# Kernel tuning notes

Hardware: AMD Instinct MI355X
Metric: run time of the kernel (lower is better)

The kernel has to match this reference:

```python
import jax, jax.numpy as jnp
import numpy as np

B, S, H = 4, 2048, 1024
NH, HD = 16, 64
WIN = 64  # window_size = min(64, seq_len)
SCALE = float(np.sqrt(HD))


def setup_inputs() -> dict:
    key = jax.random.key(0)
    ks = jax.random.split(key, 10)
    w = lambda k, shp: (jax.random.normal(k, shp, jnp.float32) * 0.02)
    return {
        "x": jax.random.normal(ks[0], (B, S, H), jnp.float32),
        "attention_mask": jnp.ones((B, S), jnp.int32),
        "Wq": w(ks[1], (H, NH * HD)), "bq": jnp.zeros((NH * HD,), jnp.float32),
        "Wk": w(ks[2], (H, NH * HD)), "bk": jnp.zeros((NH * HD,), jnp.float32),
        "Wv": w(ks[3], (H, NH * HD)), "bv": jnp.zeros((NH * HD,), jnp.float32),
        "Wo": w(ks[4], (NH * HD, H)), "bo": jnp.zeros((H,), jnp.float32),
    }


def reference(x, attention_mask, Wq, bq, Wk, bk, Wv, bv, Wo, bo):
    # projections -> [B, NH, S, HD]
    def split_heads(t):
        return t.reshape(B, S, NH, HD).transpose(0, 2, 1, 3)
    q = split_heads(x @ Wq + bq)
    k = split_heads(x @ Wk + bk)
    v = split_heads(x @ Wv + bv)

    scores = jnp.einsum("bhqd,bhkd->bhqk", q, k) / SCALE  # [B,NH,S,S]

    # local banded mask: |i - j| <= window_size // 2
    idx = jnp.arange(S)
    local = jnp.abs(idx[None, :] - idx[:, None]) <= (WIN // 2)  # [S,S]
    scores = jnp.where(local[None, None, :, :], scores, -jnp.inf)

    # padding mask: [B,1,1,S]
    scores = jnp.where(attention_mask[:, None, None, :] == 0, -jnp.inf, scores)

    probs = jax.nn.softmax(scores, axis=-1)
    probs = jnp.nan_to_num(probs)  # rows that are fully masked -> 0

    out = jnp.einsum("bhqk,bhkd->bhqd", probs, v)
    out = out.transpose(0, 2, 1, 3).reshape(B, S, NH * HD)
    return out @ Wo + bo
```

## Files before the change

kernel.cpp:

```cpp
#include <hip/hip_runtime.h>
#include <stdint.h>

typedef unsigned short u16;
typedef __attribute__((ext_vector_type(8))) short short8;
typedef __attribute__((ext_vector_type(4))) float f32x4;

#define S_LEN 2048
#define HID   1024
#define QKV_LD 3072
#define M_ROWS 8192

__device__ __forceinline__ u16 f2bf(float f) {
  unsigned u = __float_as_uint(f);
  unsigned r = (u + 0x7fffu + ((u >> 16) & 1u)) >> 16;
  return (u16)r;
}

__device__ __forceinline__ void gload16(const u16* g, u16* l) {
  __builtin_amdgcn_global_load_lds(
      (const __attribute__((address_space(1))) unsigned int*)(g),
      (__attribute__((address_space(3))) unsigned int*)(l),
      16, 0, 0);
}

__device__ __forceinline__ void wgbar() {
  asm volatile("" ::: "memory");
  __builtin_amdgcn_s_barrier();
  asm volatile("" ::: "memory");
}

__global__ __launch_bounds__(256) void prep(
    const float* __restrict__ x, u16* __restrict__ xb,
    const float* __restrict__ bq, const float* __restrict__ bk,
    const float* __restrict__ bv, float* __restrict__ bqkv,
    const float* __restrict__ Wq, const float* __restrict__ Wk,
    const float* __restrict__ Wv, const float* __restrict__ Wo,
    u16* __restrict__ wqkvt, u16* __restrict__ wot) {
  __shared__ float tile[32][33];
  const int bid = blockIdx.x;
  if (bid < 4096) {
    int i = (bid * 256 + threadIdx.x) * 8;
    float4 a = *(const float4*)(x + i);
    float4 b = *(const float4*)(x + i + 4);
    u16 t[8];
    t[0] = f2bf(a.x); t[1] = f2bf(a.y); t[2] = f2bf(a.z); t[3] = f2bf(a.w);
    t[4] = f2bf(b.x); t[5] = f2bf(b.y); t[6] = f2bf(b.z); t[7] = f2bf(b.w);
    *(short8*)(xb + i) = *(short8*)t;
    return;
  }
  if (bid == 4096) {
    for (int i = threadIdx.x; i < 3072; i += 256)
      bqkv[i] = (i < 1024) ? bq[i] : (i < 2048) ? bk[i - 1024] : bv[i - 2048];
    return;
  }
  const int wid = bid - 4097;
  const int z = wid >> 10, rem = wid & 1023;
  const float* in = (z == 0) ? Wq : (z == 1) ? Wk : (z == 2) ? Wv : Wo;
  u16* out = (z < 3) ? (wqkvt + (size_t)z * 1024 * 1024) : wot;
  int tx = threadIdx.x & 31, ty = threadIdx.x >> 5;
  int n0 = (rem & 31) * 32, k0 = (rem >> 5) * 32;
#pragma unroll
  for (int i = 0; i < 32; i += 8)
    tile[ty + i][tx] = in[(size_t)(k0 + ty + i) * 1024 + n0 + tx];
  __syncthreads();
#pragma unroll
  for (int i = 0; i < 32; i += 8)
    out[(size_t)(n0 + ty + i) * 1024 + k0 + tx] = f2bf(tile[tx][ty + i]);
}

__global__ __launch_bounds__(512, 2) void gemm_k1(
    const u16* __restrict__ A, const u16* __restrict__ Bt,
    const float* __restrict__ bias, u16* __restrict__ C) {
  constexpr int K = 1024, NT = 16, N = 3072;
  constexpr int AU = 128 * 64;
  constexpr int SLAB = 320 * 64;
  __shared__ __align__(16) u16 smem[2 * SLAB];

  const int tid = threadIdx.x;
  const int wave = tid >> 6, lane = tid & 63;
  const int qlane = lane & 15, kgrp = lane >> 4;
  const int wm = wave >> 2, wn = wave & 3;
  int wg = blockIdx.x;
  wg = (wg & 7) * 128 + (wg >> 3);
  const int bm = wg >> 4, bn = wg & 15;

  const int srow = tid >> 3;
  const int sslot = (tid & 7) ^ (srow & 7);
  uint32_t gA[2], gB[3];
#pragma unroll
  for (int u = 0; u < 2; ++u)
    gA[u] = (uint32_t)((bm * 128 + u * 64 + srow) * K + sslot * 8);
#pragma unroll
  for (int u = 0; u < 3; ++u)
    gB[u] = (uint32_t)((bn * 192 + u * 64 + srow) * K + sslot * 8);

  auto stgA = [&](int t, int u) {
    gload16(A + (size_t)gA[u] + t * 64, &smem[(t & 1) * SLAB + u * 4096 + tid * 8]);
  };
  auto stgB = [&](int t, int u) {
    gload16(Bt + (size_t)gB[u] + t * 64, &smem[(t & 1) * SLAB + AU + u * 4096 + tid * 8]);
  };

  const int key7 = qlane & 7;
  int aaddr[4], baddr[3];
#pragma unroll
  for (int mf = 0; mf < 4; ++mf)
    aaddr[mf] = (wm * 64 + mf * 16 + qlane) * 64;
#pragma unroll
  for (int nf = 0; nf < 3; ++nf)
    baddr[nf] = AU + (wn * 48 + nf * 16 + qlane) * 64;

  f32x4 acc[4][3] = {};
  short8 af[4][2], bf[2][2];

  stgA(0, 0); stgA(0, 1);
  stgB(0, 0); stgB(0, 1); stgB(0, 2);
  stgA(1, 0); stgA(1, 1);
  asm volatile("s_waitcnt vmcnt(2)" ::: "memory");
  wgbar();

  for (int t = 0; t < NT; ++t) {
    const u16* bp = &smem[(t & 1) * SLAB];

#pragma unroll
    for (int mf = 0; mf < 4; ++mf)
#pragma unroll
      for (int kk = 0; kk < 2; ++kk)
        af[mf][kk] = *(const short8*)&bp[aaddr[mf] + (((kk * 4 + kgrp) ^ key7) * 8)];
#pragma unroll
    for (int nf = 0; nf < 2; ++nf)
#pragma unroll
      for (int kk = 0; kk < 2; ++kk)
        bf[nf][kk] = *(const short8*)&bp[baddr[nf] + (((kk * 4 + kgrp) ^ key7) * 8)];
    if (t + 1 < NT) { stgB(t + 1, 0); stgB(t + 1, 1); stgB(t + 1, 2); }
    wgbar();
    asm volatile("s_waitcnt lgkmcnt(0)" ::: "memory");
    __builtin_amdgcn_s_setprio(1);
#pragma unroll
    for (int mf = 0; mf < 4; ++mf)
#pragma unroll
      for (int nf = 0; nf < 2; ++nf)
#pragma unroll
        for (int kk = 0; kk < 2; ++kk)
          acc[mf][nf] = __builtin_amdgcn_mfma_f32_16x16x32_bf16(
              af[mf][kk], bf[nf][kk], acc[mf][nf], 0, 0, 0);
    __builtin_amdgcn_s_setprio(0);
    wgbar();

#pragma unroll
    for (int kk = 0; kk < 2; ++kk)
      bf[0][kk] = *(const short8*)&bp[baddr[2] + (((kk * 4 + kgrp) ^ key7) * 8)];
    if (t + 2 < NT) { stgA(t + 2, 0); stgA(t + 2, 1); }
    wgbar();
    asm volatile("s_waitcnt lgkmcnt(0)" ::: "memory");
    __builtin_amdgcn_s_setprio(1);
#pragma unroll
    for (int mf = 0; mf < 4; ++mf)
#pragma unroll
      for (int kk = 0; kk < 2; ++kk)
        acc[mf][2] = __builtin_amdgcn_mfma_f32_16x16x32_bf16(
            af[mf][kk], bf[0][kk], acc[mf][2], 0, 0, 0);
    __builtin_amdgcn_s_setprio(0);
    if (t + 2 < NT)      asm volatile("s_waitcnt vmcnt(2)" ::: "memory");
    else if (t + 1 < NT) asm volatile("s_waitcnt vmcnt(0)" ::: "memory");
    if (t + 1 < NT) wgbar();
  }

#pragma unroll
  for (int nf = 0; nf < 3; ++nf) {
    int col = bn * 192 + wn * 48 + nf * 16 + qlane;
    float bv = bias[col];
#pragma unroll
    for (int mf = 0; mf < 4; ++mf) {
      int row0 = bm * 128 + wm * 64 + mf * 16 + kgrp * 4;
#pragma unroll
      for (int r = 0; r < 4; ++r)
        C[(size_t)(row0 + r) * N + col] = f2bf(acc[mf][nf][r] + bv);
    }
  }
}

__global__ __launch_bounds__(256, 2) void gemm_k2(
    const u16* __restrict__ A, const u16* __restrict__ Bt,
    const float* __restrict__ bias, float* __restrict__ C) {
  constexpr int K = 1024, NT = 16, N = 1024;
  constexpr int AU = 128 * 64;
  constexpr int SLAB = 256 * 64;
  __shared__ __align__(16) u16 smem[2 * SLAB];

  const int tid = threadIdx.x;
  const int wave = tid >> 6, lane = tid & 63;
  const int qlane = lane & 15, kgrp = lane >> 4;
  const int wm = wave >> 1, wn = wave & 1;
  int wg = blockIdx.x;
  wg = (wg & 7) * 64 + (wg >> 3);
  const int bm = wg >> 3, bn = wg & 7;

  const int srow = tid >> 3;
  const int sslot = (tid & 7) ^ (srow & 7);
  uint32_t gA[4], gB[4];
#pragma unroll
  for (int u = 0; u < 4; ++u) {
    gA[u] = (uint32_t)((bm * 128 + u * 32 + srow) * K + sslot * 8);
    gB[u] = (uint32_t)((bn * 128 + u * 32 + srow) * K + sslot * 8);
  }
  auto stgA = [&](int t, int u) {
    gload16(A + (size_t)gA[u] + t * 64, &smem[(t & 1) * SLAB + u * 2048 + tid * 8]);
  };
  auto stgB = [&](int t, int u) {
    gload16(Bt + (size_t)gB[u] + t * 64, &smem[(t & 1) * SLAB + AU + u * 2048 + tid * 8]);
  };

  int aaddr[4], baddr[4];
#pragma unroll
  for (int f = 0; f < 4; ++f) {
    aaddr[f] = (wm * 64 + f * 16 + qlane) * 64;
    baddr[f] = AU + (wn * 64 + f * 16 + qlane) * 64;
  }
  const int arow7 = (wm * 64 + qlane) & 7;
  const int brow7 = (wn * 64 + qlane) & 7;

  f32x4 acc[4][4] = {};
  short8 af[4][2], bf[2][2];

#pragma unroll
  for (int u = 0; u < 4; ++u) stgA(0, u);
#pragma unroll
  for (int u = 0; u < 4; ++u) stgB(0, u);
#pragma unroll
  for (int u = 0; u < 4; ++u) stgA(1, u);
  stgB(1, 0); stgB(1, 2);
  asm volatile("s_waitcnt vmcnt(6)" ::: "memory");
  wgbar();

  for (int t = 0; t < NT; ++t) {
    const u16* bp = &smem[(t & 1) * SLAB];

#pragma unroll
    for (int mf = 0; mf < 4; ++mf)
#pragma unroll
      for (int kk = 0; kk < 2; ++kk)
        af[mf][kk] = *(const short8*)&bp[aaddr[mf] + (((kk * 4 + kgrp) ^ arow7) * 8)];
#pragma unroll
    for (int nf = 0; nf < 2; ++nf)
#pragma unroll
      for (int kk = 0; kk < 2; ++kk)
        bf[nf][kk] = *(const short8*)&bp[baddr[nf] + (((kk * 4 + kgrp) ^ brow7) * 8)];
    if (t + 1 < NT) { stgB(t + 1, 1); stgB(t + 1, 3); }
    wgbar();
    asm volatile("s_waitcnt lgkmcnt(0)" ::: "memory");
    __builtin_amdgcn_s_setprio(1);
#pragma unroll
    for (int mf = 0; mf < 4; ++mf)
#pragma unroll
      for (int nf = 0; nf < 2; ++nf)
#pragma unroll
        for (int kk = 0; kk < 2; ++kk)
          acc[mf][nf] = __builtin_amdgcn_mfma_f32_16x16x32_bf16(
              af[mf][kk], bf[nf][kk], acc[mf][nf], 0, 0, 0);
    __builtin_amdgcn_s_setprio(0);
    wgbar();

#pragma unroll
    for (int nf = 0; nf < 2; ++nf)
#pragma unroll
      for (int kk = 0; kk < 2; ++kk)
        bf[nf][kk] = *(const short8*)&bp[baddr[nf + 2] + (((kk * 4 + kgrp) ^ brow7) * 8)];
    if (t + 2 < NT) {
      stgA(t + 2, 0); stgA(t + 2, 1); stgA(t + 2, 2); stgA(t + 2, 3);
      stgB(t + 2, 0); stgB(t + 2, 2);
    }
    wgbar();
    asm volatile("s_waitcnt lgkmcnt(0)" ::: "memory");
    __builtin_amdgcn_s_setprio(1);
#pragma unroll
    for (int mf = 0; mf < 4; ++mf)
#pragma unroll
      for (int nf = 0; nf < 2; ++nf)
#pragma unroll
        for (int kk = 0; kk < 2; ++kk)
          acc[mf][nf + 2] = __builtin_amdgcn_mfma_f32_16x16x32_bf16(
              af[mf][kk], bf[nf][kk], acc[mf][nf + 2], 0, 0, 0);
    __builtin_amdgcn_s_setprio(0);
    if (t + 2 < NT)      asm volatile("s_waitcnt vmcnt(6)" ::: "memory");
    else if (t + 1 < NT) asm volatile("s_waitcnt vmcnt(0)" ::: "memory");
    if (t + 1 < NT) wgbar();
  }

#pragma unroll
  for (int nf = 0; nf < 4; ++nf) {
    int col = bn * 128 + wn * 64 + nf * 16 + qlane;
    float bv = bias[col];
#pragma unroll
    for (int mf = 0; mf < 4; ++mf) {
      int row0 = bm * 128 + wm * 64 + mf * 16 + kgrp * 4;
#pragma unroll
      for (int r = 0; r < 4; ++r)
        C[(size_t)(row0 + r) * N + col] = acc[mf][nf][r] + bv;
    }
  }
}

__global__ __launch_bounds__(256, 2) void attn_local(
    const u16* __restrict__ qkv, const int* __restrict__ amask,
    u16* __restrict__ aout) {
  __shared__ __align__(16) u16 Kl[192][72];
  __shared__ __align__(16) u16 Vt[64][200];
  __shared__ __align__(16) u16 Pl[4][32][104];

  const int tid = threadIdx.x, wave = tid >> 6, lane = tid & 63;
  const int qlane = lane & 15, kgrp = lane >> 4;
  const int rbz = blockIdx.x;
  const int bz = (rbz & 7) * 128 + (rbz >> 3);
  const int qt = bz & 15, h = (bz >> 4) & 15, b = bz >> 8;
  const int qs0 = qt * 128;
  const int jt = qs0 - 32;
  const size_t rbase = (size_t)b * S_LEN;

  {
    const int r0 = tid >> 3, c0 = (tid & 7) * 8;
#pragma unroll
    for (int p = 0; p < 6; ++p) {
      int row = p * 32 + r0;
      int j = jt + row;
      u16 kv[8], vv[8];
      if (j >= 0 && j < S_LEN) {
        const u16* kp = qkv + (rbase + j) * QKV_LD + HID + h * 64 + c0;
        *(short8*)kv = *(const short8*)kp;
        *(short8*)vv = *(const short8*)(kp + HID);
      } else {
#pragma unroll
        for (int q = 0; q < 8; ++q) { kv[q] = 0; vv[q] = 0; }
      }
      *(short8*)&Kl[row][c0] = *(short8*)kv;
#pragma unroll
      for (int q = 0; q < 8; ++q) Vt[c0 + q][row] = vv[q];
    }
  }

  short8 qf[2][2];
#pragma unroll
  for (int mf = 0; mf < 2; ++mf)
#pragma unroll
    for (int kk = 0; kk < 2; ++kk)
      qf[mf][kk] = *(const short8*)(qkv +
          (rbase + qs0 + wave * 32 + mf * 16 + qlane) * QKV_LD +
          h * 64 + kk * 32 + kgrp * 8);

  __syncthreads();

  f32x4 sc[2][6] = {};
#pragma unroll
  for (int kk = 0; kk < 2; ++kk) {
    short8 kf[6];
#pragma unroll
    for (int nf = 0; nf < 6; ++nf)
      kf[nf] = *(const short8*)&Kl[wave * 32 + nf * 16 + qlane][kk * 32 + kgrp * 8];
#pragma unroll
    for (int mf = 0; mf < 2; ++mf)
#pragma unroll
      for (int nf = 0; nf < 6; ++nf)
        sc[mf][nf] = __builtin_amdgcn_mfma_f32_16x16x32_bf16(
            qf[mf][kk], kf[nf], sc[mf][nf], 0, 0, 0);
  }

  int jcol[6], mv[6];
#pragma unroll
  for (int nf = 0; nf < 6; ++nf) {
    int j = jt + wave * 32 + nf * 16 + qlane;
    jcol[nf] = j;
    mv[nf] = (j >= 0 && j < S_LEN) ? amask[rbase + j] : 0;
  }

  float inv[2][4];
#pragma unroll
  for (int mf = 0; mf < 2; ++mf) {
    const int irow0 = qs0 + wave * 32 + mf * 16 + kgrp * 4;
    float mx[4] = {-1e30f, -1e30f, -1e30f, -1e30f};
#pragma unroll
    for (int r = 0; r < 4; ++r) {
      int i = irow0 + r;
#pragma unroll
      for (int nf = 0; nf < 6; ++nf) {
        int d = i - jcol[nf];
        if (mv[nf] && d >= -32 && d <= 32) mx[r] = fmaxf(mx[r], sc[mf][nf][r]);
      }
    }
#pragma unroll
    for (int m = 1; m < 16; m <<= 1)
#pragma unroll
      for (int r = 0; r < 4; ++r)
        mx[r] = fmaxf(mx[r], __shfl_xor(mx[r], m));
    float sm[4] = {0.f, 0.f, 0.f, 0.f};
#pragma unroll
    for (int r = 0; r < 4; ++r) {
      int i = irow0 + r;
#pragma unroll
      for (int nf = 0; nf < 6; ++nf) {
        int d = i - jcol[nf];
        bool val = mv[nf] && d >= -32 && d <= 32;
        float p = val ? __expf((sc[mf][nf][r] - mx[r]) * 0.125f) : 0.f;
        sc[mf][nf][r] = p;
        sm[r] += p;
      }
    }
#pragma unroll
    for (int m = 1; m < 16; m <<= 1)
#pragma unroll
      for (int r = 0; r < 4; ++r)
        sm[r] += __shfl_xor(sm[r], m);
#pragma unroll
    for (int r = 0; r < 4; ++r)
      inv[mf][r] = sm[r] > 0.f ? 1.f / sm[r] : 0.f;
#pragma unroll
    for (int nf = 0; nf < 6; ++nf)
#pragma unroll
      for (int r = 0; r < 4; ++r)
        Pl[wave][mf * 16 + kgrp * 4 + r][nf * 16 + qlane] = f2bf(sc[mf][nf][r]);
  }
  __syncthreads();

  f32x4 oc[2][4] = {};
#pragma unroll
  for (int ks = 0; ks < 3; ++ks) {
    short8 pa[2], vb[4];
#pragma unroll
    for (int mf = 0; mf < 2; ++mf)
      pa[mf] = *(const short8*)&Pl[wave][mf * 16 + qlane][ks * 32 + kgrp * 8];
#pragma unroll
    for (int nf = 0; nf < 4; ++nf)
      vb[nf] = *(const short8*)&Vt[nf * 16 + qlane][wave * 32 + ks * 32 + kgrp * 8];
#pragma unroll
    for (int mf = 0; mf < 2; ++mf)
#pragma unroll
      for (int nf = 0; nf < 4; ++nf)
        oc[mf][nf] = __builtin_amdgcn_mfma_f32_16x16x32_bf16(
            pa[mf], vb[nf], oc[mf][nf], 0, 0, 0);
  }

#pragma unroll
  for (int mf = 0; mf < 2; ++mf)
#pragma unroll
    for (int nf = 0; nf < 4; ++nf)
#pragma unroll
      for (int r = 0; r < 4; ++r) {
        size_t row = rbase + qs0 + wave * 32 + mf * 16 + kgrp * 4 + r;
        aout[row * HID + h * 64 + nf * 16 + qlane] =
            f2bf(oc[mf][nf][r] * inv[mf][r]);
      }
}

extern "C" void kernel_launch(void* const* d_in, const int* in_sizes, int n_in,
                              void* d_out, int out_size, void* d_ws, size_t ws_size,
                              hipStream_t stream) {
  const float* x  = (const float*)d_in[0];
  const int* amask = (const int*)d_in[1];
  const float* Wq = (const float*)d_in[2];
  const float* bq = (const float*)d_in[3];
  const float* Wk = (const float*)d_in[4];
  const float* bk = (const float*)d_in[5];
  const float* Wv = (const float*)d_in[6];
  const float* bv = (const float*)d_in[7];
  const float* Wo = (const float*)d_in[8];
  const float* bo = (const float*)d_in[9];
  float* out = (float*)d_out;

  char* w = (char*)d_ws;
  u16* xb    = (u16*)w;   w += (size_t)M_ROWS * HID * 2;
  u16* wqkvt = (u16*)w;   w += (size_t)3072 * 1024 * 2;
  u16* wot   = (u16*)w;   w += (size_t)1024 * 1024 * 2;
  float* bqkv = (float*)w; w += 3072 * 4 + 256;
  u16* qkv   = (u16*)w;   w += (size_t)M_ROWS * 3072 * 2;
  u16* aout  = (u16*)w;   w += (size_t)M_ROWS * HID * 2;

  prep<<<8193, 256, 0, stream>>>(x, xb, bq, bk, bv, bqkv,
                                 Wq, Wk, Wv, Wo, wqkvt, wot);
  gemm_k1<<<1024, 512, 0, stream>>>(xb, wqkvt, bqkv, qkv);
  attn_local<<<1024, 256, 0, stream>>>(qkv, amask, aout);
  gemm_k2<<<512, 256, 0, stream>>>(aout, wot, bo, out);
}
```

Measured before the change: 112.5 us.

## Enlarge QKV GEMM block tile to 256x192 with 4x2 wave layout

The QKV projection GEMM now computes a 256x192 output tile per workgroup instead of 128x192. Its 8 waves are arranged 4x2, and each wave owns a 64x96 sub-tile. The K-step is split into four MFMA phases using half-width fragments, and A staging grows to four loads per tile. This raises data reuse per LDS load and halves the grid to 512 blocks. In exchange it uses more LDS, with 448-row slabs double-buffered (about 114KB), which may limit occupancy to one block per CU. It also adds barriers and raises accumulator register pressure.

```diff
diff --git a/kernel.cpp b/kernel.cpp
--- a/kernel.cpp
+++ b/kernel.cpp
@@ -72,24 +72,24 @@
     const u16* __restrict__ A, const u16* __restrict__ Bt,
     const float* __restrict__ bias, u16* __restrict__ C) {
   constexpr int K = 1024, NT = 16, N = 3072;
-  constexpr int AU = 128 * 64;
-  constexpr int SLAB = 320 * 64;
+  constexpr int AU = 256 * 64;
+  constexpr int SLAB = 448 * 64;
   __shared__ __align__(16) u16 smem[2 * SLAB];
 
   const int tid = threadIdx.x;
   const int wave = tid >> 6, lane = tid & 63;
   const int qlane = lane & 15, kgrp = lane >> 4;
-  const int wm = wave >> 2, wn = wave & 3;
+  const int wm = wave >> 1, wn = wave & 1;
   int wg = blockIdx.x;
-  wg = (wg & 7) * 128 + (wg >> 3);
+  wg = (wg & 7) * 64 + (wg >> 3);
   const int bm = wg >> 4, bn = wg & 15;
 
   const int srow = tid >> 3;
   const int sslot = (tid & 7) ^ (srow & 7);
-  uint32_t gA[2], gB[3];
-#pragma unroll
-  for (int u = 0; u < 2; ++u)
-    gA[u] = (uint32_t)((bm * 128 + u * 64 + srow) * K + sslot * 8);
+  uint32_t gA[4], gB[3];
+#pragma unroll
+  for (int u = 0; u < 4; ++u)
+    gA[u] = (uint32_t)((bm * 256 + u * 64 + srow) * K + sslot * 8);
 #pragma unroll
   for (int u = 0; u < 3; ++u)
     gB[u] = (uint32_t)((bn * 192 + u * 64 + srow) * K + sslot * 8);
@@ -102,21 +102,26 @@
   };
 
   const int key7 = qlane & 7;
-  int aaddr[4], baddr[3];
+  const int s0 = (kgrp ^ key7) * 8;
+  const int s1 = ((4 + kgrp) ^ key7) * 8;
+  int aaddr[4], baddr[6];
 #pragma unroll
   for (int mf = 0; mf < 4; ++mf)
     aaddr[mf] = (wm * 64 + mf * 16 + qlane) * 64;
 #pragma unroll
-  for (int nf = 0; nf < 3; ++nf)
-    baddr[nf] = AU + (wn * 48 + nf * 16 + qlane) * 64;
-
-  f32x4 acc[4][3] = {};
-  short8 af[4][2], bf[2][2];
-
-  stgA(0, 0); stgA(0, 1);
-  stgB(0, 0); stgB(0, 1); stgB(0, 2);
-  stgA(1, 0); stgA(1, 1);
-  asm volatile("s_waitcnt vmcnt(2)" ::: "memory");
+  for (int nf = 0; nf < 6; ++nf)
+    baddr[nf] = AU + (wn * 96 + nf * 16 + qlane) * 64;
+
+  f32x4 acc[4][6] = {};
+  short8 af[4], bf[3];
+
+#pragma unroll
+  for (int u = 0; u < 4; ++u) stgA(0, u);
+#pragma unroll
+  for (int u = 0; u < 3; ++u) stgB(0, u);
+#pragma unroll
+  for (int u = 0; u < 4; ++u) stgA(1, u);
+  asm volatile("s_waitcnt vmcnt(4)" ::: "memory");
   wgbar();
 
   for (int t = 0; t < NT; ++t) {
@@ -124,14 +129,10 @@
 
 #pragma unroll
     for (int mf = 0; mf < 4; ++mf)
-#pragma unroll
-      for (int kk = 0; kk < 2; ++kk)
-        af[mf][kk] = *(const short8*)&bp[aaddr[mf] + (((kk * 4 + kgrp) ^ key7) * 8)];
-#pragma unroll
-    for (int nf = 0; nf < 2; ++nf)
-#pragma unroll
-      for (int kk = 0; kk < 2; ++kk)
-        bf[nf][kk] = *(const short8*)&bp[baddr[nf] + (((kk * 4 + kgrp) ^ key7) * 8)];
+      af[mf] = *(const short8*)&bp[aaddr[mf] + s0];
+#pragma unroll
+    for (int nf = 0; nf < 3; ++nf)
+      bf[nf] = *(const short8*)&bp[baddr[nf] + s0];
     if (t + 1 < NT) { stgB(t + 1, 0); stgB(t + 1, 1); stgB(t + 1, 2); }
     wgbar();
     asm volatile("s_waitcnt lgkmcnt(0)" ::: "memory");
@@ -139,40 +140,71 @@
 #pragma unroll
     for (int mf = 0; mf < 4; ++mf)
 #pragma unroll
-      for (int nf = 0; nf < 2; ++nf)
-#pragma unroll
-        for (int kk = 0; kk < 2; ++kk)
-          acc[mf][nf] = __builtin_amdgcn_mfma_f32_16x16x32_bf16(
-              af[mf][kk], bf[nf][kk], acc[mf][nf], 0, 0, 0);
+      for (int nf = 0; nf < 3; ++nf)
+        acc[mf][nf] = __builtin_amdgcn_mfma_f32_16x16x32_bf16(
+            af[mf], bf[nf], acc[mf][nf], 0, 0, 0);
     __builtin_amdgcn_s_setprio(0);
     wgbar();
 
 #pragma unroll
-    for (int kk = 0; kk < 2; ++kk)
-      bf[0][kk] = *(const short8*)&bp[baddr[2] + (((kk * 4 + kgrp) ^ key7) * 8)];
-    if (t + 2 < NT) { stgA(t + 2, 0); stgA(t + 2, 1); }
+    for (int nf = 0; nf < 3; ++nf)
+      bf[nf] = *(const short8*)&bp[baddr[nf + 3] + s0];
     wgbar();
     asm volatile("s_waitcnt lgkmcnt(0)" ::: "memory");
     __builtin_amdgcn_s_setprio(1);
 #pragma unroll
     for (int mf = 0; mf < 4; ++mf)
 #pragma unroll
-      for (int kk = 0; kk < 2; ++kk)
-        acc[mf][2] = __builtin_amdgcn_mfma_f32_16x16x32_bf16(
-            af[mf][kk], bf[0][kk], acc[mf][2], 0, 0, 0);
+      for (int nf = 0; nf < 3; ++nf)
+        acc[mf][nf + 3] = __builtin_amdgcn_mfma_f32_16x16x32_bf16(
+            af[mf], bf[nf], acc[mf][nf + 3], 0, 0, 0);
     __builtin_amdgcn_s_setprio(0);
-    if (t + 2 < NT)      asm volatile("s_waitcnt vmcnt(2)" ::: "memory");
+    wgbar();
+
+#pragma unroll
+    for (int mf = 0; mf < 4; ++mf)
+      af[mf] = *(const short8*)&bp[aaddr[mf] + s1];
+#pragma unroll
+    for (int nf = 0; nf < 3; ++nf)
+      bf[nf] = *(const short8*)&bp[baddr[nf] + s1];
+    wgbar();
+    asm volatile("s_waitcnt lgkmcnt(0)" ::: "memory");
+    __builtin_amdgcn_s_setprio(1);
+#pragma unroll
+    for (int mf = 0; mf < 4; ++mf)
+#pragma unroll
+      for (int nf = 0; nf < 3; ++nf)
+        acc[mf][nf] = __builtin_amdgcn_mfma_f32_16x16x32_bf16(
+            af[mf], bf[nf], acc[mf][nf], 0, 0, 0);
+    __builtin_amdgcn_s_setprio(0);
+    wgbar();
+
+#pragma unroll
+    for (int nf = 0; nf < 3; ++nf)
+      bf[nf] = *(const short8*)&bp[baddr[nf + 3] + s1];
+    if (t + 2 < NT) { stgA(t + 2, 0); stgA(t + 2, 1); stgA(t + 2, 2); stgA(t + 2, 3); }
+    wgbar();
+    asm volatile("s_waitcnt lgkmcnt(0)" ::: "memory");
+    __builtin_amdgcn_s_setprio(1);
+#pragma unroll
+    for (int mf = 0; mf < 4; ++mf)
+#pragma unroll
+      for (int nf = 0; nf < 3; ++nf)
+        acc[mf][nf + 3] = __builtin_amdgcn_mfma_f32_16x16x32_bf16(
+            af[mf], bf[nf], acc[mf][nf + 3], 0, 0, 0);
+    __builtin_amdgcn_s_setprio(0);
+    if (t + 2 < NT)      asm volatile("s_waitcnt vmcnt(4)" ::: "memory");
     else if (t + 1 < NT) asm volatile("s_waitcnt vmcnt(0)" ::: "memory");
     if (t + 1 < NT) wgbar();
   }
 
 #pragma unroll
-  for (int nf = 0; nf < 3; ++nf) {
-    int col = bn * 192 + wn * 48 + nf * 16 + qlane;
+  for (int nf = 0; nf < 6; ++nf) {
+    int col = bn * 192 + wn * 96 + nf * 16 + qlane;
     float bv = bias[col];
 #pragma unroll
     for (int mf = 0; mf < 4; ++mf) {
-      int row0 = bm * 128 + wm * 64 + mf * 16 + kgrp * 4;
+      int row0 = bm * 256 + wm * 64 + mf * 16 + kgrp * 4;
 #pragma unroll
       for (int r = 0; r < 4; ++r)
         C[(size_t)(row0 + r) * N + col] = f2bf(acc[mf][nf][r] + bv);
@@ -475,7 +507,7 @@
 
   prep<<<8193, 256, 0, stream>>>(x, xb, bq, bk, bv, bqkv,
                                  Wq, Wk, Wv, Wo, wqkvt, wot);
-  gemm_k1<<<1024, 512, 0, stream>>>(xb, wqkvt, bqkv, qkv);
+  gemm_k1<<<512, 512, 0, stream>>>(xb, wqkvt, bqkv, qkv);
   attn_local<<<1024, 256, 0, stream>>>(qkv, amask, aout);
   gemm_k2<<<512, 256, 0, stream>>>(aout, wot, bo, out);
 }
```

Result: slower. 118.5 us (+5.3%).
